# Optimization experiments

Hardware: AMD Instinct MI355X
Metric: run time of the kernel (lower is better)

Reference implementation:

```python
import jax, jax.numpy as jnp
import numpy as np

B, S, HID = 4, 1024, 1024
H = 16
D = HID // H  # 64
SPARSITY = 0.9  # keep prob = 0.1


def setup_inputs() -> dict:
    key = jax.random.key(0)
    ks = jax.random.split(key, 11)
    sc = 1.0 / np.sqrt(HID)
    x = jax.random.normal(ks[0], (B, S, HID), dtype=jnp.float32)
    Wq = jax.random.normal(ks[1], (HID, HID), dtype=jnp.float32) * sc
    bq = jnp.zeros((HID,), dtype=jnp.float32)
    Wk = jax.random.normal(ks[2], (HID, HID), dtype=jnp.float32) * sc
    bk = jnp.zeros((HID,), dtype=jnp.float32)
    Wv = jax.random.normal(ks[3], (HID, HID), dtype=jnp.float32) * sc
    bv = jnp.zeros((HID,), dtype=jnp.float32)
    Wo = jax.random.normal(ks[4], (HID, HID), dtype=jnp.float32) * sc
    bo = jnp.zeros((HID,), dtype=jnp.float32)
    temperature = jnp.ones((H, 1, 1), dtype=jnp.float32)
    # training-mode random sparsity mask: rand > sparsity -> keep (True)
    sparse_mask = jax.random.uniform(ks[5], (B, H, S, S)) > SPARSITY
    return {"x": x, "Wq": Wq, "bq": bq, "Wk": Wk, "bk": bk, "Wv": Wv,
            "bv": bv, "Wo": Wo, "bo": bo, "temperature": temperature,
            "sparse_mask": sparse_mask}


def reference(x, Wq, bq, Wk, bk, Wv, bv, Wo, bo, temperature, sparse_mask):
    b, s, _ = x.shape
    def split_heads(t):
        return t.reshape(b, s, H, D).transpose(0, 2, 1, 3)  # [B,H,S,D]
    q = split_heads(x @ Wq + bq)
    k = split_heads(x @ Wk + bk)
    v = split_heads(x @ Wv + bv)
    scores = jnp.einsum('bhqd,bhkd->bhqk', q, k) / np.sqrt(D)
    scores = scores * temperature  # [H,1,1] broadcasts over [B,H,S,S]
    scores = jnp.where(sparse_mask, scores, -jnp.inf)
    attn = jax.nn.softmax(scores, axis=-1)
    out = jnp.einsum('bhqk,bhkd->bhqd', attn, v)
    out = out.transpose(0, 2, 1, 3).reshape(b, s, HID)
    return out @ Wo + bo
```

## Files before the change

kernel.cpp:

```cpp
#include <hip/hip_runtime.h>

typedef unsigned short u16;
typedef short short8 __attribute__((ext_vector_type(8)));
typedef float f32x4 __attribute__((ext_vector_type(4)));
typedef float float4v __attribute__((ext_vector_type(4)));
typedef u16 u16x4 __attribute__((ext_vector_type(4)));
typedef unsigned uint2v __attribute__((ext_vector_type(2)));
typedef unsigned long long u64;

__device__ __forceinline__ u16 f2bf(float f) {
  union { float f; unsigned u; } v; v.f = f;
  unsigned r = v.u + 0x7FFFu + ((v.u >> 16) & 1u);
  return (u16)(r >> 16);
}

__device__ __forceinline__ unsigned cvtpk(float lo, float hi) {
  unsigned r;
  asm("v_cvt_pk_bf16_f32 %0, %1, %2" : "=v"(r) : "v"(lo), "v"(hi));
  return r;
}

__device__ __forceinline__ void gload16(const void* g, void* l) {
  __builtin_amdgcn_global_load_lds(
      (const __attribute__((address_space(1))) void*)g,
      (__attribute__((address_space(3))) void*)l, 16, 0, 0);
}

union PackSS { unsigned u[4]; short8 s; };

__global__ __launch_bounds__(256)
void prep_kernel(const void* __restrict__ mask, u64* __restrict__ bits,
                 const float* __restrict__ x, u16* __restrict__ xb,
                 const float* __restrict__ W0, const float* __restrict__ W1,
                 const float* __restrict__ W2, const float* __restrict__ W3,
                 u16* __restrict__ Wt) {
  __shared__ float t[32][33];
  __shared__ int sf;
  const int bid = blockIdx.x;
  if (bid < 4096) {
    if (threadIdx.x == 0) sf = 0;
    __syncthreads();
    {
      uint4 v = ((const uint4*)mask)[threadIdx.x];
      unsigned xs[4] = {v.x, v.y, v.z, v.w};
      int f = 0;
#pragma unroll
      for (int d = 0; d < 4; ++d) {
        unsigned u = xs[d];
        if (u == 0x3F800000u) f |= 1;
        if (u & 0xFFFFFF00u) f |= 2;
        if ((d & 1) && u) f |= 4;
      }
      if (f) atomicOr(&sf, f);
    }
    __syncthreads();
    const int fl = sf;
    const int fmt = (fl & 1) ? 2 : ((fl & 2) ? 0 : ((fl & 4) ? 1 : 3));

    const int wi = bid * 256 + threadIdx.x;
    u64 b = 0;
    if (fmt == 0) {
      const uint4* mp = (const uint4*)mask + (size_t)wi * 4;
#pragma unroll
      for (int i = 0; i < 4; ++i) {
        uint4 v = mp[i];
        unsigned xw[4] = {v.x, v.y, v.z, v.w};
#pragma unroll
        for (int d = 0; d < 4; ++d)
#pragma unroll
          for (int by = 0; by < 4; ++by)
            if (xw[d] & (0xFFu << (by * 8))) b |= 1ULL << (i * 16 + d * 4 + by);
      }
    } else if (fmt != 3) {
      const uint4* mp = (const uint4*)mask + (size_t)wi * 16;
#pragma unroll
      for (int i = 0; i < 16; ++i) {
        uint4 v = mp[i];
        if (v.x) b |= 1ULL << (i * 4 + 0);
        if (v.y) b |= 1ULL << (i * 4 + 1);
        if (v.z) b |= 1ULL << (i * 4 + 2);
        if (v.w) b |= 1ULL << (i * 4 + 3);
      }
    } else {
      const uint4* mp = (const uint4*)mask + (size_t)wi * 32;
#pragma unroll
      for (int i = 0; i < 32; ++i) {
        uint4 v = mp[i];
        if (v.x | v.y) b |= 1ULL << (i * 2 + 0);
        if (v.z | v.w) b |= 1ULL << (i * 2 + 1);
      }
    }
    int bh = wi >> 14, q = (wi >> 4) & 1023, kt = wi & 15;
    bits[((size_t)bh * 16 + kt) * 1024 + q] = b;
  } else if (bid < 8192) {
    int i = ((bid - 4096) * 256 + threadIdx.x) * 4;
    float4v v = *(const float4v*)(x + i);
    u16x4 o;
    o[0] = f2bf(v[0]); o[1] = f2bf(v[1]); o[2] = f2bf(v[2]); o[3] = f2bf(v[3]);
    *(u16x4*)(xb + i) = o;
  } else {
    int i = bid - 8192;
    int z = i >> 10, rest = i & 1023;
    const float* W = (z == 0) ? W0 : (z == 1) ? W1 : (z == 2) ? W2 : W3;
    u16* out = Wt + (size_t)z * 1048576;
    int n0 = (rest & 31) * 32, k0 = (rest >> 5) * 32;
    int tx = threadIdx.x & 31, ty = threadIdx.x >> 5;
#pragma unroll
    for (int j = 0; j < 4; ++j)
      t[ty + 8 * j][tx] = W[(size_t)(k0 + ty + 8 * j) * 1024 + n0 + tx];
    __syncthreads();
#pragma unroll
    for (int j = 0; j < 4; ++j)
      out[(size_t)(n0 + ty + 8 * j) * 1024 + k0 + tx] = f2bf(t[tx][ty + 8 * j]);
  }
}

template<int BN>
__global__ __launch_bounds__(256)
void gemm_kernel(const u16* __restrict__ A,
                 const u16* __restrict__ Bt0, const u16* __restrict__ Bt1, const u16* __restrict__ Bt2,
                 const float* __restrict__ b0, const float* __restrict__ b1, const float* __restrict__ b2,
                 const float* __restrict__ temp,
                 u16* __restrict__ qb, u16* __restrict__ kb, u16* __restrict__ vT,
                 float* __restrict__ fo, int phase) {
  constexpr int K = 1024;
  constexpr int WN = BN / 2;
  constexpr int NC = WN / 16;
  __shared__ u16 As[128 * 32];
  __shared__ u16 Bs[BN * 32];
  const int tid = threadIdx.x;
  const int lane = tid & 63, w = tid >> 6;
  const int l15 = lane & 15, l4 = lane >> 4;
  const int m0 = blockIdx.x * 128, n0 = blockIdx.y * BN;
  const int z = blockIdx.z;
  const u16* Bt = (z == 0) ? Bt0 : (z == 1) ? Bt1 : Bt2;
  const float* bias = (z == 0) ? b0 : (z == 1) ? b1 : b2;
  const int wr = w >> 1, wc = w & 1;

  f32x4 acc[4][NC] = {};

  const int c0 = tid, c1 = 256 + tid;
  const u16* ga0 = A + (size_t)(m0 + (c0 >> 2)) * K + (c0 & 3) * 8;
  const u16* ga1 = A + (size_t)(m0 + (c1 >> 2)) * K + (c1 & 3) * 8;
  const u16* gb0 = Bt + (size_t)(n0 + (c0 >> 2)) * K + (c0 & 3) * 8;
  const u16* gb1 = Bt + (size_t)(n0 + (c1 >> 2)) * K + (c1 & 3) * 8;
  u16* la0 = As + c0 * 8;
  u16* la1 = As + c1 * 8;
  u16* lb0 = Bs + c0 * 8;
  u16* lb1 = Bs + c1 * 8;

  for (int kt = 0; kt < K; kt += 32) {
    gload16(ga0 + kt, la0);
    gload16(ga1 + kt, la1);
    gload16(gb0 + kt, lb0);
    if (BN == 128) gload16(gb1 + kt, lb1);
    __syncthreads();
    short8 af[4], bfr[NC];
#pragma unroll
    for (int r = 0; r < 4; ++r)
      af[r] = *(const short8*)(As + (wr * 64 + r * 16 + l15) * 32 + l4 * 8);
#pragma unroll
    for (int c = 0; c < NC; ++c)
      bfr[c] = *(const short8*)(Bs + (wc * WN + c * 16 + l15) * 32 + l4 * 8);
#pragma unroll
    for (int r = 0; r < 4; ++r)
#pragma unroll
      for (int c = 0; c < NC; ++c)
        acc[r][c] = __builtin_amdgcn_mfma_f32_16x16x32_bf16(bfr[c], af[r], acc[r][c], 0, 0, 0);
    __syncthreads();
  }

  float bvj[NC][4];
#pragma unroll
  for (int c = 0; c < NC; ++c)
#pragma unroll
    for (int j = 0; j < 4; ++j)
      bvj[c][j] = bias[n0 + wc * WN + c * 16 + l4 * 4 + j];
  const float fac = (phase == 0 && z == 0)
      ? temp[(n0 + wc * WN) >> 6] * 0.18033688011112042f : 1.0f;

#pragma unroll
  for (int r = 0; r < 4; ++r) {
    const int mm = m0 + wr * 64 + r * 16 + l15;
    const int b = mm >> 10, s = mm & 1023;
#pragma unroll
    for (int c = 0; c < NC; ++c) {
      const int n = n0 + wc * WN + c * 16 + l4 * 4;
      if (phase == 1) {
        float4v o;
#pragma unroll
        for (int j = 0; j < 4; ++j) o[j] = acc[r][c][j] + bvj[c][j];
        *(float4v*)(fo + (size_t)mm * 1024 + n) = o;
      } else if (z == 2) {
#pragma unroll
        for (int j = 0; j < 4; ++j)
          vT[((size_t)b * 1024 + n + j) * 1024 + s] = f2bf(acc[r][c][j] + bvj[c][j]);
      } else {
        unsigned lo = cvtpk((acc[r][c][0] + bvj[c][0]) * fac, (acc[r][c][1] + bvj[c][1]) * fac);
        unsigned hi = cvtpk((acc[r][c][2] + bvj[c][2]) * fac, (acc[r][c][3] + bvj[c][3]) * fac);
        unsigned o2[2] = {lo, hi};
        int hh = n >> 6, d = n & 63;
        u16* dst = (z == 0) ? qb : kb;
        *(unsigned long long*)(dst + ((((size_t)b * 16 + hh) * 1024 + s) * 64 + d)) =
            *(unsigned long long*)o2;
      }
    }
  }
}

__device__ __forceinline__ void softmax_reg(f32x4* s, u64 wcur, float& m, float& l,
                                            f32x4* oacc, int l4,
                                            PackSS& p0, PackSS& p1) {
  float mt = fmaxf(fmaxf(s[0][0], s[0][1]), fmaxf(s[0][2], s[0][3]));
#pragma unroll
  for (int cb = 1; cb < 4; ++cb)
    mt = fmaxf(mt, fmaxf(fmaxf(s[cb][0], s[cb][1]), fmaxf(s[cb][2], s[cb][3])));
  mt = fmaxf(mt, __shfl_xor(mt, 16));
  mt = fmaxf(mt, __shfl_xor(mt, 32));
  if (!__all(mt <= m + 8.f)) {
    float mnew = fmaxf(m, mt);
    float al = exp2f(m - mnew);
    l *= al;
#pragma unroll
    for (int db = 0; db < 4; ++db) oacc[db] *= al;
    m = mnew;
  }
  unsigned hws[4] = {(unsigned)wcur, (unsigned)(wcur >> 16),
                     (unsigned)(wcur >> 32), (unsigned)(wcur >> 48)};
  float rs = 0.f;
#pragma unroll
  for (int cb = 0; cb < 4; ++cb) {
#pragma unroll
    for (int j = 0; j < 4; ++j) {
      float p = exp2f(s[cb][j] - m);
      p = ((hws[cb] >> (l4 * 4 + j)) & 1) ? p : 0.f;
      rs += p;
      s[cb][j] = p;
    }
  }
  rs += __shfl_xor(rs, 16);
  rs += __shfl_xor(rs, 32);
  l += rs;
  p0.u[0] = cvtpk(s[0][0], s[0][1]); p0.u[1] = cvtpk(s[0][2], s[0][3]);
  p0.u[2] = cvtpk(s[1][0], s[1][1]); p0.u[3] = cvtpk(s[1][2], s[1][3]);
  p1.u[0] = cvtpk(s[2][0], s[2][1]); p1.u[1] = cvtpk(s[2][2], s[2][3]);
  p1.u[2] = cvtpk(s[3][0], s[3][1]); p1.u[3] = cvtpk(s[3][2], s[3][3]);
}

__global__ __launch_bounds__(256, 3)
void attn_kernel(const u16* __restrict__ qb, const u16* __restrict__ kb,
                 const u16* __restrict__ vT, const u64* __restrict__ mbits,
                 u16* __restrict__ oh) {
  __shared__ u16 Ks[2][64 * 64];
  __shared__ u16 Vs[2][64 * 64];
  const int tid = threadIdx.x, lane = tid & 63, w = tid >> 6;
  const int l15 = lane & 15, l4 = lane >> 4;
  const int id = blockIdx.x;
  const int xcd = id & 7;
  const int bh = xcd * 8 + ((id >> 3) & 7), qx = id >> 6;
  const int b = bh >> 4, h = bh & 15;
  const int q0 = qx * 128 + w * 32;
  const u16* qp = qb + ((size_t)bh * 1024 + q0) * 64;
  const u16* kp = kb + (size_t)bh * 1024 * 64;
  const u16* vp = vT + (size_t)bh * 64 * 1024;

  const int L0 = tid, L1 = tid + 256;
  const int r0 = L0 >> 3, c0 = ((L0 & 7) ^ (r0 & 7)) * 8;
  const int r1 = L1 >> 3, c1 = ((L1 & 7) ^ (r1 & 7)) * 8;
  const int swz8 = (l15 & 7) << 3;
  const int vswz = l15 & 7;

  int koff[4], vr[4], ke0, ke1, ve[2][2];
#pragma unroll
  for (int cb = 0; cb < 4; ++cb) koff[cb] = (cb * 16 + l15) * 64;
#pragma unroll
  for (int db = 0; db < 4; ++db) vr[db] = (db * 16 + l15) * 64;
  ke0 = (l4 * 8) ^ swz8;
  ke1 = (32 + l4 * 8) ^ swz8;
#pragma unroll
  for (int kg = 0; kg < 2; ++kg) {
    ve[kg][0] = (((4 * kg + (l4 >> 1)) ^ vswz) << 3) + (l4 & 1) * 4;
    ve[kg][1] = (((4 * kg + 2 + (l4 >> 1)) ^ vswz) << 3) + (l4 & 1) * 4;
  }

  short8 qa0 = *(const short8*)(qp + (size_t)l15 * 64 + l4 * 8);
  short8 qa1 = *(const short8*)(qp + (size_t)l15 * 64 + 32 + l4 * 8);
  short8 qb0 = *(const short8*)(qp + (size_t)(16 + l15) * 64 + l4 * 8);
  short8 qb1 = *(const short8*)(qp + (size_t)(16 + l15) * 64 + 32 + l4 * 8);

  float mA = -1e30f, lA = 0.f, mB = -1e30f, lB = 0.f;
  f32x4 oA[4] = {}, oB[4] = {};

  const u64* mb = mbits + (size_t)bh * 16 * 1024 + q0 + l15;
  u64 wA = mb[0], wB = mb[16];

  gload16(kp + (size_t)r0 * 64 + c0, &Ks[0][L0 * 8]);
  gload16(kp + (size_t)r1 * 64 + c1, &Ks[0][L1 * 8]);
  gload16(vp + (size_t)r0 * 1024 + c0, &Vs[0][L0 * 8]);
  gload16(vp + (size_t)r1 * 1024 + c1, &Vs[0][L1 * 8]);

  for (int t = 0; t < 16; ++t) {
    const int buf = t & 1;
    __syncthreads();

    if (t < 15) {
      const int k1 = (t + 1) * 64;
      gload16(kp + (size_t)(k1 + r0) * 64 + c0, &Ks[buf ^ 1][L0 * 8]);
      gload16(kp + (size_t)(k1 + r1) * 64 + c1, &Ks[buf ^ 1][L1 * 8]);
      gload16(vp + (size_t)r0 * 1024 + k1 + c0, &Vs[buf ^ 1][L0 * 8]);
      gload16(vp + (size_t)r1 * 1024 + k1 + c1, &Vs[buf ^ 1][L1 * 8]);
    }
    u64 wAn = 0, wBn = 0;
    if (t < 15) { wAn = mb[(t + 1) * 1024]; wBn = mb[(t + 1) * 1024 + 16]; }

    const u16* kbase = Ks[buf];
    f32x4 sa[4] = {}, sb[4] = {};
    __builtin_amdgcn_s_setprio(1);
#pragma unroll
    for (int cb = 0; cb < 4; ++cb) {
      short8 kf0 = *(const short8*)(kbase + koff[cb] + ke0);
      short8 kf1 = *(const short8*)(kbase + koff[cb] + ke1);
      sa[cb] = __builtin_amdgcn_mfma_f32_16x16x32_bf16(kf0, qa0, sa[cb], 0, 0, 0);
      sa[cb] = __builtin_amdgcn_mfma_f32_16x16x32_bf16(kf1, qa1, sa[cb], 0, 0, 0);
      sb[cb] = __builtin_amdgcn_mfma_f32_16x16x32_bf16(kf0, qb0, sb[cb], 0, 0, 0);
      sb[cb] = __builtin_amdgcn_mfma_f32_16x16x32_bf16(kf1, qb1, sb[cb], 0, 0, 0);
    }
    __builtin_amdgcn_s_setprio(0);

    PackSS pa0, pa1, pb0, pb1;
    softmax_reg(sa, wA, mA, lA, oA, l4, pa0, pa1);
    softmax_reg(sb, wB, mB, lB, oB, l4, pb0, pb1);

    const u16* vbase = Vs[buf];
    __builtin_amdgcn_s_setprio(1);
#pragma unroll
    for (int kg = 0; kg < 2; ++kg) {
#pragma unroll
      for (int db = 0; db < 4; ++db) {
        uint2v v0 = *(const uint2v*)(vbase + vr[db] + ve[kg][0]);
        uint2v v1 = *(const uint2v*)(vbase + vr[db] + ve[kg][1]);
        PackSS vf;
        vf.u[0] = v0[0]; vf.u[1] = v0[1]; vf.u[2] = v1[0]; vf.u[3] = v1[1];
        oA[db] = __builtin_amdgcn_mfma_f32_16x16x32_bf16(
            vf.s, kg ? pa1.s : pa0.s, oA[db], 0, 0, 0);
        oB[db] = __builtin_amdgcn_mfma_f32_16x16x32_bf16(
            vf.s, kg ? pb1.s : pb0.s, oB[db], 0, 0, 0);
      }
    }
    __builtin_amdgcn_s_setprio(0);
    wA = wAn; wB = wBn;
  }

  float rlA = 1.f / lA, rlB = 1.f / lB;
  u16* orowA = oh + ((size_t)b * 1024 + q0 + l15) * 1024 + h * 64;
  u16* orowB = oh + ((size_t)b * 1024 + q0 + 16 + l15) * 1024 + h * 64;
#pragma unroll
  for (int db = 0; db < 4; ++db) {
    unsigned a0 = cvtpk(oA[db][0] * rlA, oA[db][1] * rlA);
    unsigned a1 = cvtpk(oA[db][2] * rlA, oA[db][3] * rlA);
    unsigned b0 = cvtpk(oB[db][0] * rlB, oB[db][1] * rlB);
    unsigned b1 = cvtpk(oB[db][2] * rlB, oB[db][3] * rlB);
    unsigned oAa[2] = {a0, a1}, oBb[2] = {b0, b1};
    *(unsigned long long*)(orowA + db * 16 + l4 * 4) = *(unsigned long long*)oAa;
    *(unsigned long long*)(orowB + db * 16 + l4 * 4) = *(unsigned long long*)oBb;
  }
}

extern "C" void kernel_launch(void* const* d_in, const int* in_sizes, int n_in,
                              void* d_out, int out_size, void* d_ws, size_t ws_size,
                              hipStream_t stream) {
  const float* x = (const float*)d_in[0];
  const float* Wq = (const float*)d_in[1];
  const float* bq = (const float*)d_in[2];
  const float* Wk = (const float*)d_in[3];
  const float* bk = (const float*)d_in[4];
  const float* Wv = (const float*)d_in[5];
  const float* bv = (const float*)d_in[6];
  const float* Wo = (const float*)d_in[7];
  const float* bo = (const float*)d_in[8];
  const float* temp = (const float*)d_in[9];
  const void* mask = (const void*)d_in[10];

  char* ws = (char*)d_ws;
  u16* xb = (u16*)(ws + 256);
  u16* Wt = xb + (size_t)4 * 1024 * 1024;
  u16* qbuf = Wt + (size_t)4 * 1024 * 1024;
  u16* kbuf = qbuf + (size_t)4 * 1024 * 1024;
  u16* vTb = kbuf + (size_t)4 * 1024 * 1024;
  u64* mbits = (u64*)(vTb + (size_t)4 * 1024 * 1024);
  u16* oh = xb;

  prep_kernel<<<12288, 256, 0, stream>>>(mask, mbits, x, xb, Wq, Wk, Wv, Wo, Wt);
  gemm_kernel<128><<<dim3(32, 8, 3), 256, 0, stream>>>(
      xb, Wt, Wt + 1048576, Wt + 2 * 1048576,
      bq, bk, bv, temp, qbuf, kbuf, vTb, nullptr, 0);
  attn_kernel<<<512, 256, 0, stream>>>(qbuf, kbuf, vTb, mbits, oh);
  gemm_kernel<64><<<dim3(32, 16, 1), 256, 0, stream>>>(
      oh, Wt + 3 * 1048576, nullptr, nullptr,
      bo, nullptr, nullptr, temp, nullptr, nullptr, nullptr, (float*)d_out, 1);
}
```

Baseline: 190.1 us.

## Double-buffer GEMM LDS tiles with 64-wide K and XOR-swizzled layout

The projection GEMM kernel now loads 64-wide K slices into two LDS buffers. The next tile's global-to-LDS loads are issued before the current tile's MFMAs run, and there is one barrier per iteration instead of two. Columns within each LDS row are XOR-swizzled by row to reduce bank conflicts on the short8 fragment reads. This aims to hide global load latency and cut barrier overhead, at the cost of four times the LDS footprint, which may lower occupancy.

Result: slower. 194.9 us (+2.5%).

```diff
diff --git a/kernel.cpp b/kernel.cpp
--- a/kernel.cpp
+++ b/kernel.cpp
@@ -123,11 +123,11 @@
                  const float* __restrict__ temp,
                  u16* __restrict__ qb, u16* __restrict__ kb, u16* __restrict__ vT,
                  float* __restrict__ fo, int phase) {
-  constexpr int K = 1024;
   constexpr int WN = BN / 2;
   constexpr int NC = WN / 16;
-  __shared__ u16 As[128 * 32];
-  __shared__ u16 Bs[BN * 32];
+  constexpr int BLOADS = BN / 32;
+  __shared__ u16 As[2][128 * 64];
+  __shared__ u16 Bs[2][BN * 64];
   const int tid = threadIdx.x;
   const int lane = tid & 63, w = tid >> 6;
   const int l15 = lane & 15, l4 = lane >> 4;
@@ -139,35 +139,61 @@
 
   f32x4 acc[4][NC] = {};
 
-  const int c0 = tid, c1 = 256 + tid;
-  const u16* ga0 = A + (size_t)(m0 + (c0 >> 2)) * K + (c0 & 3) * 8;
-  const u16* ga1 = A + (size_t)(m0 + (c1 >> 2)) * K + (c1 & 3) * 8;
-  const u16* gb0 = Bt + (size_t)(n0 + (c0 >> 2)) * K + (c0 & 3) * 8;
-  const u16* gb1 = Bt + (size_t)(n0 + (c1 >> 2)) * K + (c1 & 3) * 8;
-  u16* la0 = As + c0 * 8;
-  u16* la1 = As + c1 * 8;
-  u16* lb0 = Bs + c0 * 8;
-  u16* lb1 = Bs + c1 * 8;
-
-  for (int kt = 0; kt < K; kt += 32) {
-    gload16(ga0 + kt, la0);
-    gload16(ga1 + kt, la1);
-    gload16(gb0 + kt, lb0);
-    if (BN == 128) gload16(gb1 + kt, lb1);
+  int srow[4], scg[4];
+#pragma unroll
+  for (int i = 0; i < 4; ++i) {
+    int c = tid + 256 * i;
+    srow[i] = c >> 3;
+    scg[i] = ((c & 7) ^ (srow[i] & 7)) * 8;
+  }
+
+  const int ke0 = ((l4) ^ (l15 & 7)) * 8;
+  const int ke1 = ((4 + l4) ^ (l15 & 7)) * 8;
+  int arow[4], brow[NC];
+#pragma unroll
+  for (int r = 0; r < 4; ++r) arow[r] = (wr * 64 + r * 16 + l15) * 64;
+#pragma unroll
+  for (int c = 0; c < NC; ++c) brow[c] = (wc * WN + c * 16 + l15) * 64;
+
+#pragma unroll
+  for (int i = 0; i < 4; ++i)
+    gload16(A + (size_t)(m0 + srow[i]) * 1024 + scg[i], &As[0][(tid + 256 * i) * 8]);
+#pragma unroll
+  for (int i = 0; i < BLOADS; ++i)
+    gload16(Bt + (size_t)(n0 + srow[i]) * 1024 + scg[i], &Bs[0][(tid + 256 * i) * 8]);
+
+  for (int t = 0; t < 16; ++t) {
+    const int buf = t & 1;
     __syncthreads();
-    short8 af[4], bfr[NC];
-#pragma unroll
-    for (int r = 0; r < 4; ++r)
-      af[r] = *(const short8*)(As + (wr * 64 + r * 16 + l15) * 32 + l4 * 8);
-#pragma unroll
-    for (int c = 0; c < NC; ++c)
-      bfr[c] = *(const short8*)(Bs + (wc * WN + c * 16 + l15) * 32 + l4 * 8);
-#pragma unroll
-    for (int r = 0; r < 4; ++r)
-#pragma unroll
-      for (int c = 0; c < NC; ++c)
-        acc[r][c] = __builtin_amdgcn_mfma_f32_16x16x32_bf16(bfr[c], af[r], acc[r][c], 0, 0, 0);
-    __syncthreads();
+
+    if (t < 15) {
+      const int kt = (t + 1) * 64;
+#pragma unroll
+      for (int i = 0; i < 4; ++i)
+        gload16(A + (size_t)(m0 + srow[i]) * 1024 + kt + scg[i],
+                &As[buf ^ 1][(tid + 256 * i) * 8]);
+#pragma unroll
+      for (int i = 0; i < BLOADS; ++i)
+        gload16(Bt + (size_t)(n0 + srow[i]) * 1024 + kt + scg[i],
+                &Bs[buf ^ 1][(tid + 256 * i) * 8]);
+    }
+
+    const u16* ab = As[buf];
+    const u16* bb = Bs[buf];
+#pragma unroll
+    for (int kk = 0; kk < 2; ++kk) {
+      const int ke = kk ? ke1 : ke0;
+      short8 af[4], bf[NC];
+#pragma unroll
+      for (int r = 0; r < 4; ++r) af[r] = *(const short8*)(ab + arow[r] + ke);
+#pragma unroll
+      for (int c = 0; c < NC; ++c) bf[c] = *(const short8*)(bb + brow[c] + ke);
+#pragma unroll
+      for (int r = 0; r < 4; ++r)
+#pragma unroll
+        for (int c = 0; c < NC; ++c)
+          acc[r][c] = __builtin_amdgcn_mfma_f32_16x16x32_bf16(bf[c], af[r], acc[r][c], 0, 0, 0);
+    }
   }
 
   float bvj[NC][4];
```

## Move mask bit-packing into the QKV GEMM epilogue to overlap with compute

Applied to the files above, without the earlier changes.

The mask-to-bitmask packing moves out of the prep kernel and into the tail of the QKV projection GEMM. Each of the 768 GEMM blocks packs up to six slices of the mask after its epilogue. The aim is to hide the memory-bound mask read behind the compute-bound GEMM running on other CUs, and to shrink the prep launch. The GEMM also gets a launch_bounds occupancy hint of 3 blocks per SM, which may cap registers and cause spills, and the GEMM tail gets longer.

After: 167.1 us. 1.14x faster.

```diff
diff --git a/kernel.cpp b/kernel.cpp
--- a/kernel.cpp
+++ b/kernel.cpp
@@ -29,80 +29,23 @@
 union PackSS { unsigned u[4]; short8 s; };
 
 __global__ __launch_bounds__(256)
-void prep_kernel(const void* __restrict__ mask, u64* __restrict__ bits,
-                 const float* __restrict__ x, u16* __restrict__ xb,
-                 const float* __restrict__ W0, const float* __restrict__ W1,
-                 const float* __restrict__ W2, const float* __restrict__ W3,
-                 u16* __restrict__ Wt) {
+void cvt_kernel(const float* __restrict__ x, u16* __restrict__ xb,
+                const float* __restrict__ W0, const float* __restrict__ W1,
+                const float* __restrict__ W2, const float* __restrict__ W3,
+                u16* __restrict__ Wt) {
   __shared__ float t[32][33];
-  __shared__ int sf;
   const int bid = blockIdx.x;
   if (bid < 4096) {
-    if (threadIdx.x == 0) sf = 0;
-    __syncthreads();
-    {
-      uint4 v = ((const uint4*)mask)[threadIdx.x];
-      unsigned xs[4] = {v.x, v.y, v.z, v.w};
-      int f = 0;
-#pragma unroll
-      for (int d = 0; d < 4; ++d) {
-        unsigned u = xs[d];
-        if (u == 0x3F800000u) f |= 1;
-        if (u & 0xFFFFFF00u) f |= 2;
-        if ((d & 1) && u) f |= 4;
-      }
-      if (f) atomicOr(&sf, f);
-    }
-    __syncthreads();
-    const int fl = sf;
-    const int fmt = (fl & 1) ? 2 : ((fl & 2) ? 0 : ((fl & 4) ? 1 : 3));
-
-    const int wi = bid * 256 + threadIdx.x;
-    u64 b = 0;
-    if (fmt == 0) {
-      const uint4* mp = (const uint4*)mask + (size_t)wi * 4;
-#pragma unroll
-      for (int i = 0; i < 4; ++i) {
-        uint4 v = mp[i];
-        unsigned xw[4] = {v.x, v.y, v.z, v.w};
-#pragma unroll
-        for (int d = 0; d < 4; ++d)
-#pragma unroll
-          for (int by = 0; by < 4; ++by)
-            if (xw[d] & (0xFFu << (by * 8))) b |= 1ULL << (i * 16 + d * 4 + by);
-      }
-    } else if (fmt != 3) {
-      const uint4* mp = (const uint4*)mask + (size_t)wi * 16;
-#pragma unroll
-      for (int i = 0; i < 16; ++i) {
-        uint4 v = mp[i];
-        if (v.x) b |= 1ULL << (i * 4 + 0);
-        if (v.y) b |= 1ULL << (i * 4 + 1);
-        if (v.z) b |= 1ULL << (i * 4 + 2);
-        if (v.w) b |= 1ULL << (i * 4 + 3);
-      }
-    } else {
-      const uint4* mp = (const uint4*)mask + (size_t)wi * 32;
-#pragma unroll
-      for (int i = 0; i < 32; ++i) {
-        uint4 v = mp[i];
-        if (v.x | v.y) b |= 1ULL << (i * 2 + 0);
-        if (v.z | v.w) b |= 1ULL << (i * 2 + 1);
-      }
-    }
-    int bh = wi >> 14, q = (wi >> 4) & 1023, kt = wi & 15;
-    bits[((size_t)bh * 16 + kt) * 1024 + q] = b;
-  } else if (bid < 8192) {
-    int i = ((bid - 4096) * 256 + threadIdx.x) * 4;
+    int i = (bid * 256 + threadIdx.x) * 4;
     float4v v = *(const float4v*)(x + i);
     u16x4 o;
     o[0] = f2bf(v[0]); o[1] = f2bf(v[1]); o[2] = f2bf(v[2]); o[3] = f2bf(v[3]);
     *(u16x4*)(xb + i) = o;
   } else {
-    int i = bid - 8192;
+    int i = bid - 4096;
     int z = i >> 10, rest = i & 1023;
     const float* W = (z == 0) ? W0 : (z == 1) ? W1 : (z == 2) ? W2 : W3;
-    u16* out = Wt + (size_t)z * 1048576;
+    u16* outw = Wt + (size_t)z * 1048576;
     int n0 = (rest & 31) * 32, k0 = (rest >> 5) * 32;
     int tx = threadIdx.x & 31, ty = threadIdx.x >> 5;
 #pragma unroll
@@ -111,23 +54,25 @@
     __syncthreads();
 #pragma unroll
     for (int j = 0; j < 4; ++j)
-      out[(size_t)(n0 + ty + 8 * j) * 1024 + k0 + tx] = f2bf(t[tx][ty + 8 * j]);
+      outw[(size_t)(n0 + ty + 8 * j) * 1024 + k0 + tx] = f2bf(t[tx][ty + 8 * j]);
   }
 }
 
 template<int BN>
-__global__ __launch_bounds__(256)
+__global__ __launch_bounds__(256, 3)
 void gemm_kernel(const u16* __restrict__ A,
                  const u16* __restrict__ Bt0, const u16* __restrict__ Bt1, const u16* __restrict__ Bt2,
                  const float* __restrict__ b0, const float* __restrict__ b1, const float* __restrict__ b2,
                  const float* __restrict__ temp,
                  u16* __restrict__ qb, u16* __restrict__ kb, u16* __restrict__ vT,
-                 float* __restrict__ fo, int phase) {
+                 float* __restrict__ fo, int phase,
+                 const void* __restrict__ mask, u64* __restrict__ bits) {
   constexpr int K = 1024;
   constexpr int WN = BN / 2;
   constexpr int NC = WN / 16;
   __shared__ u16 As[128 * 32];
   __shared__ u16 Bs[BN * 32];
+  __shared__ int sf;
   const int tid = threadIdx.x;
   const int lane = tid & 63, w = tid >> 6;
   const int l15 = lane & 15, l4 = lane >> 4;
@@ -204,6 +149,67 @@
         *(unsigned long long*)(dst + ((((size_t)b * 16 + hh) * 1024 + s) * 64 + d)) =
             *(unsigned long long*)o2;
       }
+    }
+  }
+
+  if (phase == 0) {
+    if (tid == 0) sf = 0;
+    __syncthreads();
+    {
+      uint4 v = ((const uint4*)mask)[tid];
+      unsigned xs[4] = {v.x, v.y, v.z, v.w};
+      int f = 0;
+#pragma unroll
+      for (int d = 0; d < 4; ++d) {
+        unsigned u = xs[d];
+        if (u == 0x3F800000u) f |= 1;
+        if (u & 0xFFFFFF00u) f |= 2;
+        if ((d & 1) && u) f |= 4;
+      }
+      if (f) atomicOr(&sf, f);
+    }
+    __syncthreads();
+    const int fl = sf;
+    const int fmt = (fl & 1) ? 2 : ((fl & 2) ? 0 : ((fl & 4) ? 1 : 3));
+
+    const int gb = z * 256 + blockIdx.y * 32 + blockIdx.x;
+    for (int it = 0; it < 6; ++it) {
+      const int wi = (it * 768 + gb) * 256 + tid;
+      if (wi >= 1048576) break;
+      u64 b = 0;
+      if (fmt == 0) {
+        const uint4* mp = (const uint4*)mask + (size_t)wi * 4;
+#pragma unroll
+        for (int i = 0; i < 4; ++i) {
+          uint4 v = mp[i];
+          unsigned xw[4] = {v.x, v.y, v.z, v.w};
+#pragma unroll
+          for (int d = 0; d < 4; ++d)
+#pragma unroll
+            for (int by = 0; by < 4; ++by)
+              if (xw[d] & (0xFFu << (by * 8))) b |= 1ULL << (i * 16 + d * 4 + by);
+        }
+      } else if (fmt != 3) {
+        const uint4* mp = (const uint4*)mask + (size_t)wi * 16;
+#pragma unroll
+        for (int i = 0; i < 16; ++i) {
+          uint4 v = mp[i];
+          if (v.x) b |= 1ULL << (i * 4 + 0);
+          if (v.y) b |= 1ULL << (i * 4 + 1);
+          if (v.z) b |= 1ULL << (i * 4 + 2);
+          if (v.w) b |= 1ULL << (i * 4 + 3);
+        }
+      } else {
+        const uint4* mp = (const uint4*)mask + (size_t)wi * 32;
+#pragma unroll
+        for (int i = 0; i < 32; ++i) {
+          uint4 v = mp[i];
+          if (v.x | v.y) b |= 1ULL << (i * 2 + 0);
+          if (v.z | v.w) b |= 1ULL << (i * 2 + 1);
+        }
+      }
+      int bh = wi >> 14, q = (wi >> 4) & 1023, kt = wi & 15;
+      bits[((size_t)bh * 16 + kt) * 1024 + q] = b;
     }
   }
 }
@@ -390,12 +396,13 @@
   u64* mbits = (u64*)(vTb + (size_t)4 * 1024 * 1024);
   u16* oh = xb;
 
-  prep_kernel<<<12288, 256, 0, stream>>>(mask, mbits, x, xb, Wq, Wk, Wv, Wo, Wt);
+  cvt_kernel<<<8192, 256, 0, stream>>>(x, xb, Wq, Wk, Wv, Wo, Wt);
   gemm_kernel<128><<<dim3(32, 8, 3), 256, 0, stream>>>(
       xb, Wt, Wt + 1048576, Wt + 2 * 1048576,
-      bq, bk, bv, temp, qbuf, kbuf, vTb, nullptr, 0);
+      bq, bk, bv, temp, qbuf, kbuf, vTb, nullptr, 0, mask, mbits);
   attn_kernel<<<512, 256, 0, stream>>>(qbuf, kbuf, vTb, mbits, oh);
   gemm_kernel<64><<<dim3(32, 16, 1), 256, 0, stream>>>(
       oh, Wt + 3 * 1048576, nullptr, nullptr,
-      bo, nullptr, nullptr, temp, nullptr, nullptr, nullptr, (float*)d_out, 1);
-}
+      bo, nullptr, nullptr, temp, nullptr, nullptr, nullptr,
+      (float*)d_out, 1, nullptr, nullptr);
+}
```
